# Kernel optimization log

Measured on AMD Instinct MI355X. Metric: run time of the kernel, lower is better.

## Reference

```python
import jax, jax.numpy as jnp
import numpy as np

NUM_HEADS = 32
HEAD_DIM = 128
HIDDEN = 4096
SEQ = 2048
BATCH = 1


def rotate_half(x):
    x1, x2 = jnp.split(x, 2, axis=-1)
    return jnp.concatenate((-x2, x1), axis=-1)


def rope_cos_sin(seq_len, dim, dtype=jnp.float32):
    inv_freq = 1.0 / (10000.0 ** (jnp.arange(0, dim, 2, dtype=jnp.float32) / dim))
    t = jnp.arange(seq_len, dtype=jnp.float32)
    freqs = jnp.einsum('i,j->ij', t, inv_freq)          # [S, dim/2]
    emb = jnp.concatenate((freqs, freqs), axis=-1)       # [S, dim]
    return jnp.cos(emb).astype(dtype), jnp.sin(emb).astype(dtype)


def setup_inputs() -> dict:
    key = jax.random.key(0)
    ks = jax.random.split(key, 6)
    s = 1.0 / np.sqrt(HIDDEN)
    return {
        'hidden_states': jax.random.normal(ks[0], (BATCH, SEQ, HIDDEN), jnp.float32),
        'attention_mask': jnp.ones((BATCH, SEQ), jnp.int32),
        'Wq': jax.random.normal(ks[1], (HIDDEN, HIDDEN), jnp.float32) * s,
        'Wk': jax.random.normal(ks[2], (HIDDEN, HIDDEN), jnp.float32) * s,
        'Wv': jax.random.normal(ks[3], (HIDDEN, HIDDEN), jnp.float32) * s,
        'Wo': jax.random.normal(ks[4], (HIDDEN, HIDDEN), jnp.float32) * s,
        'latent_queries': jax.random.normal(ks[5], (1, SEQ, HIDDEN), jnp.float32) * s,
    }


def reference(hidden_states, attention_mask, Wq, Wk, Wv, Wo, latent_queries):
    B, S, H = hidden_states.shape
    hd = HEAD_DIM
    scaling = hd ** -0.5

    def split_heads(x):  # [B,S,H] -> [B,nh,S,hd]
        return x.reshape(B, S, NUM_HEADS, hd).transpose(0, 2, 1, 3)

    k = split_heads(hidden_states @ Wk.T)
    v = split_heads(hidden_states @ Wv.T)

    cos, sin = rope_cos_sin(S, hd, hidden_states.dtype)  # [S,hd]
    cos = cos[None, None]
    sin = sin[None, None]
    k = k * cos + rotate_half(k) * sin  # rotated q is dead code in the original

    latents = jnp.broadcast_to(latent_queries[:, :S, :], (B, S, H))
    latent_q = split_heads(latents @ Wq.T)

    scores = jnp.einsum('bhqd,bhkd->bhqk', latent_q, k) * scaling
    mask = attention_mask[:, None, None, :] == 0
    scores = jnp.where(mask, -jnp.inf, scores)
    attn = jax.nn.softmax(scores.astype(jnp.float32), axis=-1).astype(hidden_states.dtype)
    # dropout is identity in eval mode
    out = jnp.einsum('bhqk,bhkd->bhqd', attn, v)
    out = out.transpose(0, 2, 1, 3).reshape(B, S, H)
    return out @ Wo.T
```

## Files before the change

kernel.cpp:

```cpp
#include <hip/hip_runtime.h>
#include <cstdint>
#include <type_traits>

typedef short bf16x8 __attribute__((ext_vector_type(8)));
typedef float f32x4 __attribute__((ext_vector_type(4)));

__device__ __forceinline__ ushort f2bf(float f) {
  union { float f; uint32_t u; } v; v.f = f;
  return (ushort)((v.u + 0x7fffu + ((v.u >> 16) & 1u)) >> 16);
}
__device__ __forceinline__ float bf2f(ushort u) {
  union { uint32_t u; float f; } v; v.u = ((uint32_t)u) << 16;
  return v.f;
}
__device__ __forceinline__ uint32_t pkbf(float x, float y) {
  uint32_t ux = (__float_as_uint(x) + 0x8000u) >> 16;
  uint32_t uy = (__float_as_uint(y) + 0x8000u) & 0xffff0000u;
  return ux | uy;
}

__device__ __forceinline__ void gld16(const void* g, void* l) {
  __builtin_amdgcn_global_load_lds(
      (__attribute__((address_space(1))) void*)(g),
      (__attribute__((address_space(3))) void*)(l), 16, 0, 0);
}

__device__ __forceinline__ uint4 ld8(const ushort* p) { return *(const uint4*)p; }
__device__ __forceinline__ uint4 ld8(const float* p) {
  float4 a = *(const float4*)p;
  float4 b = *(const float4*)(p + 4);
  uint4 r;
  r.x = pkbf(a.x, a.y); r.y = pkbf(a.z, a.w);
  r.z = pkbf(b.x, b.y); r.w = pkbf(b.z, b.w);
  return r;
}

__global__ __launch_bounds__(256) void cvt_bf16(
    const float* __restrict__ src, ushort* __restrict__ dst, int n8)
{
  int i = blockIdx.x * 256 + threadIdx.x;
  if (i >= n8) return;
  const float4* s = (const float4*)src;
  float4 a = s[2 * i], b = s[2 * i + 1];
  uint4 r;
  r.x = pkbf(a.x, a.y); r.y = pkbf(a.z, a.w);
  r.z = pkbf(b.x, b.y); r.w = pkbf(b.z, b.w);
  ((uint4*)dst)[i] = r;
}


#define BARw() __builtin_amdgcn_s_barrier()
#define LGKMW() do { asm volatile("s_waitcnt lgkmcnt(0)" ::: "memory"); \
                     __builtin_amdgcn_sched_barrier(0); } while (0)
#define VM6() asm volatile("s_waitcnt vmcnt(6)" ::: "memory")
#define VM0() asm volatile("s_waitcnt vmcnt(0)" ::: "memory")

__device__ __forceinline__ void stage_half8(
    const ushort* __restrict__ G, int row0, int col0,
    ushort* lds, int wave, int r4, int c8)
{
#pragma unroll
  for (int q = 0; q < 2; ++q) {
    const int si = q * 8 + wave;
    const ushort* g = G + (size_t)(row0 + (si >> 1) * 16 + r4) * 4096
                        + (col0 + (si & 1) * 32 + c8);
    gld16(g, lds + si * 512);
  }
}

__device__ __forceinline__ void read_a8(const ushort* base, int wm, int l16,
                                        int quad, bf16x8 (&a)[4][2])
{
#pragma unroll
  for (int f = 0; f < 4; ++f)
#pragma unroll
    for (int ks = 0; ks < 2; ++ks)
      a[f][ks] = *(const bf16x8*)(base + ((wm * 4 + f) * 2 + ks) * 512
                                       + l16 * 32 + quad * 8);
}

__device__ __forceinline__ void read_b8(const ushort* base, int wn, int l16,
                                        int quad, bf16x8 (&b)[2][2])
{
#pragma unroll
  for (int f = 0; f < 2; ++f)
#pragma unroll
    for (int ks = 0; ks < 2; ++ks)
      b[f][ks] = *(const bf16x8*)(base + ((wn * 2 + f) * 2 + ks) * 512
                                       + l16 * 32 + quad * 8);
}

template <int MH, int NH>
__device__ __forceinline__ void mfma_quad(const bf16x8 (&a)[4][2],
                                          const bf16x8 (&b)[2][2],
                                          f32x4 (&acc)[8][4])
{
  __builtin_amdgcn_s_setprio(1);
#pragma unroll
  for (int ks = 0; ks < 2; ++ks)
#pragma unroll
    for (int f = 0; f < 4; ++f)
#pragma unroll
      for (int g = 0; g < 2; ++g)
        acc[MH * 4 + f][NH * 2 + g] = __builtin_amdgcn_mfma_f32_16x16x32_bf16(
            a[f][ks], b[g][ks], acc[MH * 4 + f][NH * 2 + g], 0, 0, 0);
  __builtin_amdgcn_s_setprio(0);
}

__global__ __launch_bounds__(512, 2) void gemm_qkv8(
    const ushort* __restrict__ hb, const ushort* __restrict__ lb,
    const ushort* __restrict__ wkv, const ushort* __restrict__ wq,
    ushort* __restrict__ Kbf, ushort* __restrict__ Vtb, ushort* __restrict__ Qb)
{
  __shared__ __align__(16) ushort smem[65536];
#define LDSA(P, H) (smem + (P) * 32768 + (H) * 8192)
#define LDSB(P, H) (smem + (P) * 32768 + 16384 + (H) * 8192)

  const int tid  = threadIdx.x;
  const int wave = tid >> 6;
  const int lane = tid & 63;
  const int quad = lane >> 4;
  const int l16  = lane & 15;
  const int wm   = wave >> 2;
  const int wn   = wave & 3;
  const int r4   = lane >> 2;
  const int c8   = (lane & 3) * 8;

  const int bid = blockIdx.x;
  const int swz = (bid & 7) * 48 + (bid >> 3);
  const int xt  = swz % 48;
  const int m0  = (swz / 48) * 256;

  const ushort* Ag; const ushort* Bg; int n0;
  if (xt < 32) { Ag = hb; Bg = wkv; n0 = xt * 256; }
  else         { Ag = lb; Bg = wq;  n0 = (xt - 32) * 256; }

  f32x4 acc[8][4];
#pragma unroll
  for (int i = 0; i < 8; ++i)
#pragma unroll
    for (int j = 0; j < 4; ++j) acc[i][j] = {0.f, 0.f, 0.f, 0.f};

  bf16x8 a[4][2], b0[2][2], b1[2][2];

  stage_half8(Ag, m0,       0,  LDSA(0, 0), wave, r4, c8);
  stage_half8(Bg, n0,       0,  LDSB(0, 0), wave, r4, c8);
  stage_half8(Bg, n0 + 128, 0,  LDSB(0, 1), wave, r4, c8);
  stage_half8(Ag, m0 + 128, 0,  LDSA(0, 1), wave, r4, c8);
  stage_half8(Ag, m0,       64, LDSA(1, 0), wave, r4, c8);
  stage_half8(Bg, n0,       64, LDSB(1, 0), wave, r4, c8);
  stage_half8(Bg, n0 + 128, 64, LDSB(1, 1), wave, r4, c8);
  VM6();
  BARw();

#pragma unroll 1
  for (int t = 0; t < 64; t += 2) {
    read_a8(LDSA(0, 0), wm, l16, quad, a);
    read_b8(LDSB(0, 0), wn, l16, quad, b0);
    stage_half8(Ag, m0 + 128, (t + 1) * 64, LDSA(1, 1), wave, r4, c8);
    BARw(); LGKMW();
    mfma_quad<0, 0>(a, b0, acc);
    BARw();
    read_b8(LDSB(0, 1), wn, l16, quad, b1);
    if (t < 62) stage_half8(Ag, m0, (t + 2) * 64, LDSA(0, 0), wave, r4, c8);
    BARw(); LGKMW();
    mfma_quad<0, 1>(a, b1, acc);
    BARw();
    read_a8(LDSA(0, 1), wm, l16, quad, a);
    if (t < 62) stage_half8(Bg, n0, (t + 2) * 64, LDSB(0, 0), wave, r4, c8);
    BARw(); LGKMW();
    mfma_quad<1, 0>(a, b0, acc);
    BARw();
    if (t < 62) stage_half8(Bg, n0 + 128, (t + 2) * 64, LDSB(0, 1), wave, r4, c8);
    BARw(); LGKMW();
    mfma_quad<1, 1>(a, b1, acc);
    if (t < 62) VM6(); else VM0();
    BARw();

    read_a8(LDSA(1, 0), wm, l16, quad, a);
    read_b8(LDSB(1, 0), wn, l16, quad, b0);
    if (t < 62) stage_half8(Ag, m0 + 128, (t + 2) * 64, LDSA(0, 1), wave, r4, c8);
    BARw(); LGKMW();
    mfma_quad<0, 0>(a, b0, acc);
    BARw();
    read_b8(LDSB(1, 1), wn, l16, quad, b1);
    if (t < 61) stage_half8(Ag, m0, (t + 3) * 64, LDSA(1, 0), wave, r4, c8);
    BARw(); LGKMW();
    mfma_quad<0, 1>(a, b1, acc);
    BARw();
    read_a8(LDSA(1, 1), wm, l16, quad, a);
    if (t < 61) stage_half8(Bg, n0, (t + 3) * 64, LDSB(1, 0), wave, r4, c8);
    BARw(); LGKMW();
    mfma_quad<1, 0>(a, b0, acc);
    BARw();
    if (t < 61) stage_half8(Bg, n0 + 128, (t + 3) * 64, LDSB(1, 1), wave, r4, c8);
    BARw(); LGKMW();
    mfma_quad<1, 1>(a, b1, acc);
    if (t < 60) { VM6(); } else if (t < 62) { VM0(); }
    BARw();
  }

  const int route = (xt >= 32) ? 2 : (n0 >= 4096 ? 1 : 0);
#pragma unroll
  for (int fm = 0; fm < 8; ++fm) {
    const int rowb = m0 + (fm >> 2) * 128 + wm * 64 + (fm & 3) * 16 + quad * 4;
#pragma unroll
    for (int fn = 0; fn < 4; ++fn) {
      const int col = n0 + (fn >> 1) * 128 + wn * 32 + (fn & 1) * 16 + l16;
#pragma unroll
      for (int r = 0; r < 4; ++r) {
        const ushort val = f2bf(acc[fm][fn][r]);
        const int row = rowb + r;
        if (route == 0)      Kbf[(size_t)row * 4096 + col] = val;
        else if (route == 1) Vtb[(size_t)(col - 4096) * 2048 + row] = val;
        else                 Qb[(size_t)row * 4096 + col] = val;
      }
    }
  }
#undef LDSA
#undef LDSB
}

__global__ __launch_bounds__(256) void gemm_splitk(
    const ushort* __restrict__ A, const ushort* __restrict__ B,
    float* __restrict__ P)
{
  __shared__ __align__(16) ushort As[128 * 32];
  __shared__ __align__(16) ushort Bs[128 * 32];

  const int tid  = threadIdx.x;
  const int wave = tid >> 6;
  const int lane = tid & 63;
  const int quad = lane >> 4;
  const int l16  = lane & 15;
  const int m0 = blockIdx.y * 128;
  const int n0 = blockIdx.x * 128;
  const int K  = 4096;
  const int kb = blockIdx.z * 2048;

  const int wm = (wave & 1) * 64;
  const int wn = (wave >> 1) * 64;
  const int srow = lane >> 2;
  const int scol = (lane & 3) * 8;
  const ushort* ga0 = A + (size_t)(m0 + 32 * wave + srow) * K + scol + kb;
  const ushort* ga1 = ga0 + (size_t)16 * K;
  const ushort* gb0 = B + (size_t)(n0 + 32 * wave + srow) * K + scol + kb;
  const ushort* gb1 = gb0 + (size_t)16 * K;
  ushort* la0 = As + (2 * wave) * 512;
  ushort* la1 = As + (2 * wave + 1) * 512;
  ushort* lb0 = Bs + (2 * wave) * 512;
  ushort* lb1 = Bs + (2 * wave + 1) * 512;

  f32x4 acc[4][4];
#pragma unroll
  for (int i = 0; i < 4; i++)
#pragma unroll
    for (int j = 0; j < 4; j++) acc[i][j] = {0.f, 0.f, 0.f, 0.f};

  for (int k0 = 0; k0 < 2048; k0 += 32) {
    __syncthreads();
    gld16(ga0 + k0, la0);
    gld16(ga1 + k0, la1);
    gld16(gb0 + k0, lb0);
    gld16(gb1 + k0, lb1);
    __syncthreads();

    bf16x8 af[4], bfr[4];
#pragma unroll
    for (int i = 0; i < 4; i++) {
      af[i]  = *(const bf16x8*)(As + (wm + i * 16 + l16) * 32 + quad * 8);
      bfr[i] = *(const bf16x8*)(Bs + (wn + i * 16 + l16) * 32 + quad * 8);
    }
#pragma unroll
    for (int im = 0; im < 4; im++)
#pragma unroll
      for (int in = 0; in < 4; in++)
        acc[im][in] = __builtin_amdgcn_mfma_f32_16x16x32_bf16(
            af[im], bfr[in], acc[im][in], 0, 0, 0);
  }

  float* myP = P + (size_t)blockIdx.z * 2048 * 4096;
#pragma unroll
  for (int im = 0; im < 4; im++)
#pragma unroll
    for (int in = 0; in < 4; in++)
#pragma unroll
      for (int r = 0; r < 4; r++) {
        int row = m0 + wm + im * 16 + quad * 4 + r;
        int col = n0 + wn + in * 16 + l16;
        myP[(size_t)row * 4096 + col] = acc[im][in][r];
      }
}

__global__ __launch_bounds__(256) void reduce2(
    const float* __restrict__ P, float* __restrict__ out, int n4)
{
  int i = blockIdx.x * 256 + threadIdx.x;
  if (i >= n4) return;
  const float4* p0 = (const float4*)P;
  const float4* p1 = (const float4*)(P + (size_t)2048 * 4096);
  float4 a = p0[i], b = p1[i];
  float4 r; r.x = a.x + b.x; r.y = a.y + b.y; r.z = a.z + b.z; r.w = a.w + b.w;
  ((float4*)out)[i] = r;
}

template <bool TRANSC, typename TA, typename TB, typename TC>
__global__ __launch_bounds__(256) void gemm_bt(
    const TA* __restrict__ A, const TB* __restrict__ B,
    TC* __restrict__ C, int M, int N, int K, int ldc)
{
  __shared__ __align__(16) ushort As[128 * 32];
  __shared__ __align__(16) ushort Bs[128 * 32];

  const int tid  = threadIdx.x;
  const int wave = tid >> 6;
  const int lane = tid & 63;
  const int quad = lane >> 4;
  const int l16  = lane & 15;
  const int m0 = blockIdx.y * 128;
  const int n0 = blockIdx.x * 128;
  const int wm = (wave & 1) * 64;
  const int wn = (wave >> 1) * 64;
  const int r0 = tid >> 2;
  const int c0 = (tid & 3) * 8;

  f32x4 acc[4][4];
#pragma unroll
  for (int i = 0; i < 4; i++)
#pragma unroll
    for (int j = 0; j < 4; j++) acc[i][j] = {0.f, 0.f, 0.f, 0.f};

  const TA* aptr = A + (size_t)(m0 + r0) * K + c0;
  const TB* bptr = B + (size_t)(n0 + r0) * K + c0;

  for (int k0 = 0; k0 < K; k0 += 32) {
    uint4 av0 = ld8(aptr + k0);
    uint4 av1 = ld8(aptr + (size_t)64 * K + k0);
    uint4 bv0 = ld8(bptr + k0);
    uint4 bv1 = ld8(bptr + (size_t)64 * K + k0);
    __syncthreads();
    *(uint4*)(As + r0 * 32 + c0)        = av0;
    *(uint4*)(As + (r0 + 64) * 32 + c0) = av1;
    *(uint4*)(Bs + r0 * 32 + c0)        = bv0;
    *(uint4*)(Bs + (r0 + 64) * 32 + c0) = bv1;
    __syncthreads();

    bf16x8 af[4], bfr[4];
#pragma unroll
    for (int i = 0; i < 4; i++) {
      af[i]  = *(const bf16x8*)(As + (wm + i * 16 + l16) * 32 + quad * 8);
      bfr[i] = *(const bf16x8*)(Bs + (wn + i * 16 + l16) * 32 + quad * 8);
    }
#pragma unroll
    for (int im = 0; im < 4; im++)
#pragma unroll
      for (int in = 0; in < 4; in++)
        acc[im][in] = __builtin_amdgcn_mfma_f32_16x16x32_bf16(
            af[im], bfr[in], acc[im][in], 0, 0, 0);
  }

#pragma unroll
  for (int im = 0; im < 4; im++)
#pragma unroll
    for (int in = 0; in < 4; in++)
#pragma unroll
      for (int r = 0; r < 4; r++) {
        int row = m0 + wm + im * 16 + quad * 4 + r;
        int col = n0 + wn + in * 16 + l16;
        float fv = acc[im][in][r];
        TC val;
        if constexpr (std::is_same<TC, ushort>::value) val = f2bf(fv);
        else                                           val = fv;
        if (TRANSC) C[(size_t)col * ldc + row] = val;
        else        C[(size_t)row * ldc + col] = val;
      }
}

__global__ __launch_bounds__(256) void rope_kernel(ushort* __restrict__ Kb)
{
  int idx = blockIdx.x * 256 + threadIdx.x;
  int j  = idx & 63;
  int hs = idx >> 6;
  int s  = hs >> 5;
  float freq = expf(-0.14391156f * (float)j);
  float ang  = (float)s * freq;
  float sn, c;
  sincosf(ang, &sn, &c);
  size_t base = (size_t)hs * 128 + j;
  float k1 = bf2f(Kb[base]);
  float k2 = bf2f(Kb[base + 64]);
  Kb[base]      = f2bf(k1 * c - k2 * sn);
  Kb[base + 64] = f2bf(k2 * c + k1 * sn);
}

__global__ __launch_bounds__(256) void flash_attn(
    const ushort* __restrict__ Q, const ushort* __restrict__ Kb,
    const ushort* __restrict__ Vt, ushort* __restrict__ AO)
{
  __shared__ __align__(16) ushort Kt[128 * 128];
  __shared__ __align__(16) ushort Vs[128 * 128];
  __shared__ __align__(16) ushort Ps[4][16 * 128];

  const int tid  = threadIdx.x;
  const int wave = tid >> 6;
  const int lane = tid & 63;
  const int quad = lane >> 4;
  const int l16  = lane & 15;
  const int h  = blockIdx.y;
  const int q0 = blockIdx.x * 64 + wave * 16;
  const float scale = 0.08838834764831845f;

  bf16x8 aq[4];
#pragma unroll
  for (int kt = 0; kt < 4; kt++)
    aq[kt] = *(const bf16x8*)(Q + (size_t)(q0 + l16) * 4096 + h * 128 + kt * 32 + quad * 8);

  f32x4 Oacc[8];
#pragma unroll
  for (int dt = 0; dt < 8; dt++) Oacc[dt] = {0.f, 0.f, 0.f, 0.f};
  float m_i[4], l_i[4];
#pragma unroll
  for (int r = 0; r < 4; r++) { m_i[r] = -1e30f; l_i[r] = 0.f; }

  ushort* myP = &Ps[wave][0];

  for (int kv = 0; kv < 2048; kv += 128) {
    __syncthreads();
#pragma unroll
    for (int it = 0; it < 8; it++) {
      int i   = tid + it * 256;
      int row = i >> 4;
      int g   = i & 15;
      int sw  = (g ^ (row & 15)) * 8;
      *(uint4*)(Kt + row * 128 + sw) =
          *(const uint4*)(Kb + (size_t)(kv + row) * 4096 + h * 128 + g * 8);
      *(uint4*)(Vs + row * 128 + sw) =
          *(const uint4*)(Vt + (size_t)(h * 128 + row) * 2048 + kv + g * 8);
    }
    __syncthreads();

    f32x4 sA[8];
#pragma unroll
    for (int nt = 0; nt < 8; nt++) sA[nt] = {0.f, 0.f, 0.f, 0.f};
#pragma unroll
    for (int nt = 0; nt < 8; nt++) {
      int row = nt * 16 + l16;
#pragma unroll
      for (int kt = 0; kt < 4; kt++) {
        int g = kt * 4 + quad;
        bf16x8 bk = *(const bf16x8*)(Kt + row * 128 + ((g ^ (row & 15)) * 8));
        sA[nt] = __builtin_amdgcn_mfma_f32_16x16x32_bf16(aq[kt], bk, sA[nt], 0, 0, 0);
      }
    }

    float tmax[4];
#pragma unroll
    for (int r = 0; r < 4; r++) {
      float m = sA[0][r];
#pragma unroll
      for (int nt = 1; nt < 8; nt++) m = fmaxf(m, sA[nt][r]);
      tmax[r] = m;
    }
#pragma unroll
    for (int msk = 1; msk < 16; msk <<= 1)
#pragma unroll
      for (int r = 0; r < 4; r++)
        tmax[r] = fmaxf(tmax[r], __shfl_xor(tmax[r], msk));

    float alpha[4];
#pragma unroll
    for (int r = 0; r < 4; r++) {
      float mn = fmaxf(m_i[r], tmax[r] * scale);
      alpha[r] = __expf(m_i[r] - mn);
      m_i[r] = mn;
    }
    float rsum[4] = {0.f, 0.f, 0.f, 0.f};
#pragma unroll
    for (int nt = 0; nt < 8; nt++)
#pragma unroll
      for (int r = 0; r < 4; r++) {
        float p = __expf(sA[nt][r] * scale - m_i[r]);
        sA[nt][r] = p;
        rsum[r] += p;
      }
#pragma unroll
    for (int msk = 1; msk < 16; msk <<= 1)
#pragma unroll
      for (int r = 0; r < 4; r++) rsum[r] += __shfl_xor(rsum[r], msk);
#pragma unroll
    for (int r = 0; r < 4; r++) l_i[r] = l_i[r] * alpha[r] + rsum[r];

#pragma unroll
    for (int nt = 0; nt < 8; nt++)
#pragma unroll
      for (int r = 0; r < 4; r++) {
        int row = quad * 4 + r;
        int col = nt * 16 + l16;
        myP[row * 128 + (((col >> 3) ^ row) * 8) + (col & 7)] = f2bf(sA[nt][r]);
      }

#pragma unroll
    for (int dt = 0; dt < 8; dt++)
#pragma unroll
      for (int r = 0; r < 4; r++) Oacc[dt][r] *= alpha[r];

#pragma unroll
    for (int kt = 0; kt < 4; kt++) {
      int g = kt * 4 + quad;
      bf16x8 ap = *(const bf16x8*)(myP + l16 * 128 + ((g ^ l16) * 8));
#pragma unroll
      for (int dt = 0; dt < 8; dt++) {
        int vrow = dt * 16 + l16;
        bf16x8 bv = *(const bf16x8*)(Vs + vrow * 128 + ((g ^ (vrow & 15)) * 8));
        Oacc[dt] = __builtin_amdgcn_mfma_f32_16x16x32_bf16(ap, bv, Oacc[dt], 0, 0, 0);
      }
    }
  }

#pragma unroll
  for (int dt = 0; dt < 8; dt++)
#pragma unroll
    for (int r = 0; r < 4; r++) {
      int row = q0 + quad * 4 + r;
      int col = h * 128 + dt * 16 + l16;
      AO[(size_t)row * 4096 + col] = f2bf(Oacc[dt][r] / l_i[r]);
    }
}

extern "C" void kernel_launch(void* const* d_in, const int* in_sizes, int n_in,
                              void* d_out, int out_size, void* d_ws, size_t ws_size,
                              hipStream_t stream)
{
  const float* hidden  = (const float*)d_in[0];
  const float* Wq      = (const float*)d_in[2];
  const float* Wk      = (const float*)d_in[3];
  const float* Wv      = (const float*)d_in[4];
  const float* Wo      = (const float*)d_in[5];
  const float* latents = (const float*)d_in[6];
  float* out = (float*)d_out;

  const size_t SB = (size_t)2048 * 4096 * 2;
  char* w = (char*)d_ws;
  const int n8_act = 2048 * 4096 / 8;
  const int n8_wt  = 4096 * 4096 / 8;

  if (ws_size >= 13 * SB) {
    ushort* hb  = (ushort*)(w);
    ushort* lb  = (ushort*)(w + 1 * SB);
    ushort* wqb = (ushort*)(w + 2 * SB);
    ushort* wkv = (ushort*)(w + 4 * SB);
    ushort* wob = (ushort*)(w + 8 * SB);
    ushort* Qb  = (ushort*)(w + 10 * SB);
    ushort* Kbf = (ushort*)(w + 11 * SB);
    ushort* Vtb = (ushort*)(w + 12 * SB);
    ushort* AOb = wqb;
    float*  Pp  = (float*)(w + 4 * SB);

    cvt_bf16<<<n8_act / 256, 256, 0, stream>>>(hidden,  hb,  n8_act);
    cvt_bf16<<<n8_act / 256, 256, 0, stream>>>(latents, lb,  n8_act);
    cvt_bf16<<<n8_wt / 256, 256, 0, stream>>>(Wq, wqb, n8_wt);
    cvt_bf16<<<n8_wt / 256, 256, 0, stream>>>(Wk, wkv, n8_wt);
    cvt_bf16<<<n8_wt / 256, 256, 0, stream>>>(Wv, wkv + (size_t)4096 * 4096, n8_wt);
    cvt_bf16<<<n8_wt / 256, 256, 0, stream>>>(Wo, wob, n8_wt);

    gemm_qkv8<<<dim3(384), 512, 0, stream>>>(hb, lb, wkv, wqb, Kbf, Vtb, Qb);
    rope_kernel<<<(2048 * 32 * 64) / 256, 256, 0, stream>>>(Kbf);
    flash_attn<<<dim3(32, 32), 256, 0, stream>>>(Qb, Kbf, Vtb, AOb);
    gemm_splitk<<<dim3(32, 16, 2), 256, 0, stream>>>(AOb, wob, Pp);
    reduce2<<<(2048 * 4096 / 4 + 255) / 256, 256, 0, stream>>>(Pp, out, 2048 * 4096 / 4);
  } else {
    ushort* Qb  = (ushort*)(w);
    ushort* Kbf = (ushort*)(w + 1 * SB);
    ushort* Vtb = (ushort*)(w + 2 * SB);
    ushort* AOb = (ushort*)(w + 3 * SB);

    gemm_bt<false><<<dim3(32, 16), 256, 0, stream>>>(latents, Wq, Qb, 2048, 4096, 4096, 4096);
    gemm_bt<false><<<dim3(32, 16), 256, 0, stream>>>(hidden, Wk, Kbf, 2048, 4096, 4096, 4096);
    gemm_bt<true><<<dim3(32, 16), 256, 0, stream>>>(hidden, Wv, Vtb, 2048, 4096, 4096, 2048);
    rope_kernel<<<(2048 * 32 * 64) / 256, 256, 0, stream>>>(Kbf);
    flash_attn<<<dim3(32, 32), 256, 0, stream>>>(Qb, Kbf, Vtb, AOb);
    gemm_bt<false><<<dim3(32, 16), 256, 0, stream>>>(AOb, Wo, out, 2048, 4096, 4096, 4096);
  }
}
```

Baseline: 949.9 us.

## Reuse pipelined 256x256 GEMM for output projection and restructure flash attention

The fused QKV GEMM kernel is templated on K-iterations and mode so the output projection's split-K GEMM uses the same deep-pipelined 256x256 tile kernel instead of the simple 128x128 one. Flash attention moves to 512-thread blocks covering 128 queries and prefetches the next K/V tile into registers while computing the current one. It also raises MFMA priority and applies the lazy rescale trick, rescaling the running max and accumulators only when the max grows by more than a threshold. These changes target low MFMA utilisation and exposed global-load latency, at the cost of higher register pressure and fewer blocks for the output GEMM.

```diff
diff --git a/kernel.cpp b/kernel.cpp
--- a/kernel.cpp
+++ b/kernel.cpp
@@ -107,10 +107,12 @@
   __builtin_amdgcn_s_setprio(0);
 }
 
-__global__ __launch_bounds__(512, 2) void gemm_qkv8(
-    const ushort* __restrict__ hb, const ushort* __restrict__ lb,
-    const ushort* __restrict__ wkv, const ushort* __restrict__ wq,
-    ushort* __restrict__ Kbf, ushort* __restrict__ Vtb, ushort* __restrict__ Qb)
+template <int NT, int MODE>
+__global__ __launch_bounds__(512, 2) void gemm8(
+    const ushort* __restrict__ A0, const ushort* __restrict__ A1,
+    const ushort* __restrict__ B0, const ushort* __restrict__ B1,
+    ushort* __restrict__ O0, ushort* __restrict__ O1, ushort* __restrict__ O2,
+    float* __restrict__ PF)
 {
   __shared__ __align__(16) ushort smem[65536];
 #define LDSA(P, H) (smem + (P) * 32768 + (H) * 8192)
@@ -127,13 +129,24 @@
   const int c8   = (lane & 3) * 8;
 
   const int bid = blockIdx.x;
-  const int swz = (bid & 7) * 48 + (bid >> 3);
-  const int xt  = swz % 48;
-  const int m0  = (swz / 48) * 256;
-
-  const ushort* Ag; const ushort* Bg; int n0;
-  if (xt < 32) { Ag = hb; Bg = wkv; n0 = xt * 256; }
-  else         { Ag = lb; Bg = wq;  n0 = (xt - 32) * 256; }
+  const ushort* Ag; const ushort* Bg;
+  int m0, n0, kbase = 0, route = 0, kz = 0;
+  if constexpr (MODE == 0) {
+    const int swz = (bid & 7) * 48 + (bid >> 3);
+    const int xt  = swz % 48;
+    m0 = (swz / 48) * 256;
+    if (xt < 32) { Ag = A0; Bg = B0; n0 = xt * 256; }
+    else         { Ag = A1; Bg = B1; n0 = (xt - 32) * 256; }
+    route = (xt >= 32) ? 2 : (n0 >= 4096 ? 1 : 0);
+  } else {
+    const int swz = (bid & 7) * 32 + (bid >> 3);
+    kz = swz >> 7;
+    const int r = swz & 127;
+    m0 = (r >> 4) * 256;
+    n0 = (r & 15) * 256;
+    kbase = kz * 2048;
+    Ag = A0; Bg = B0;
+  }
 
   f32x4 acc[8][4];
 #pragma unroll
@@ -143,153 +156,102 @@
 
   bf16x8 a[4][2], b0[2][2], b1[2][2];
 
-  stage_half8(Ag, m0,       0,  LDSA(0, 0), wave, r4, c8);
-  stage_half8(Bg, n0,       0,  LDSB(0, 0), wave, r4, c8);
-  stage_half8(Bg, n0 + 128, 0,  LDSB(0, 1), wave, r4, c8);
-  stage_half8(Ag, m0 + 128, 0,  LDSA(0, 1), wave, r4, c8);
-  stage_half8(Ag, m0,       64, LDSA(1, 0), wave, r4, c8);
-  stage_half8(Bg, n0,       64, LDSB(1, 0), wave, r4, c8);
-  stage_half8(Bg, n0 + 128, 64, LDSB(1, 1), wave, r4, c8);
+  stage_half8(Ag, m0,       kbase,      LDSA(0, 0), wave, r4, c8);
+  stage_half8(Bg, n0,       kbase,      LDSB(0, 0), wave, r4, c8);
+  stage_half8(Bg, n0 + 128, kbase,      LDSB(0, 1), wave, r4, c8);
+  stage_half8(Ag, m0 + 128, kbase,      LDSA(0, 1), wave, r4, c8);
+  stage_half8(Ag, m0,       kbase + 64, LDSA(1, 0), wave, r4, c8);
+  stage_half8(Bg, n0,       kbase + 64, LDSB(1, 0), wave, r4, c8);
+  stage_half8(Bg, n0 + 128, kbase + 64, LDSB(1, 1), wave, r4, c8);
   VM6();
   BARw();
 
 #pragma unroll 1
-  for (int t = 0; t < 64; t += 2) {
+  for (int t = 0; t < NT; t += 2) {
     read_a8(LDSA(0, 0), wm, l16, quad, a);
     read_b8(LDSB(0, 0), wn, l16, quad, b0);
-    stage_half8(Ag, m0 + 128, (t + 1) * 64, LDSA(1, 1), wave, r4, c8);
+    stage_half8(Ag, m0 + 128, kbase + (t + 1) * 64, LDSA(1, 1), wave, r4, c8);
     BARw(); LGKMW();
     mfma_quad<0, 0>(a, b0, acc);
     BARw();
+
     read_b8(LDSB(0, 1), wn, l16, quad, b1);
-    if (t < 62) stage_half8(Ag, m0, (t + 2) * 64, LDSA(0, 0), wave, r4, c8);
+    if (t < NT - 2) stage_half8(Ag, m0, kbase + (t + 2) * 64, LDSA(0, 0), wave, r4, c8);
     BARw(); LGKMW();
     mfma_quad<0, 1>(a, b1, acc);
     BARw();
+
     read_a8(LDSA(0, 1), wm, l16, quad, a);
-    if (t < 62) stage_half8(Bg, n0, (t + 2) * 64, LDSB(0, 0), wave, r4, c8);
+    if (t < NT - 2) stage_half8(Bg, n0, kbase + (t + 2) * 64, LDSB(0, 0), wave, r4, c8);
     BARw(); LGKMW();
     mfma_quad<1, 0>(a, b0, acc);
     BARw();
-    if (t < 62) stage_half8(Bg, n0 + 128, (t + 2) * 64, LDSB(0, 1), wave, r4, c8);
+
+    if (t < NT - 2) stage_half8(Bg, n0 + 128, kbase + (t + 2) * 64, LDSB(0, 1), wave, r4, c8);
     BARw(); LGKMW();
     mfma_quad<1, 1>(a, b1, acc);
-    if (t < 62) VM6(); else VM0();
+    if (t < NT - 2) VM6(); else VM0();
     BARw();
 
     read_a8(LDSA(1, 0), wm, l16, quad, a);
     read_b8(LDSB(1, 0), wn, l16, quad, b0);
-    if (t < 62) stage_half8(Ag, m0 + 128, (t + 2) * 64, LDSA(0, 1), wave, r4, c8);
+    if (t < NT - 2) stage_half8(Ag, m0 + 128, kbase + (t + 2) * 64, LDSA(0, 1), wave, r4, c8);
     BARw(); LGKMW();
     mfma_quad<0, 0>(a, b0, acc);
     BARw();
+
     read_b8(LDSB(1, 1), wn, l16, quad, b1);
-    if (t < 61) stage_half8(Ag, m0, (t + 3) * 64, LDSA(1, 0), wave, r4, c8);
+    if (t < NT - 3) stage_half8(Ag, m0, kbase + (t + 3) * 64, LDSA(1, 0), wave, r4, c8);
     BARw(); LGKMW();
     mfma_quad<0, 1>(a, b1, acc);
     BARw();
+
     read_a8(LDSA(1, 1), wm, l16, quad, a);
-    if (t < 61) stage_half8(Bg, n0, (t + 3) * 64, LDSB(1, 0), wave, r4, c8);
+    if (t < NT - 3) stage_half8(Bg, n0, kbase + (t + 3) * 64, LDSB(1, 0), wave, r4, c8);
     BARw(); LGKMW();
     mfma_quad<1, 0>(a, b0, acc);
     BARw();
-    if (t < 61) stage_half8(Bg, n0 + 128, (t + 3) * 64, LDSB(1, 1), wave, r4, c8);
+
+    if (t < NT - 3) stage_half8(Bg, n0 + 128, kbase + (t + 3) * 64, LDSB(1, 1), wave, r4, c8);
     BARw(); LGKMW();
     mfma_quad<1, 1>(a, b1, acc);
-    if (t < 60) { VM6(); } else if (t < 62) { VM0(); }
-    BARw();
-  }
-
-  const int route = (xt >= 32) ? 2 : (n0 >= 4096 ? 1 : 0);
-#pragma unroll
-  for (int fm = 0; fm < 8; ++fm) {
-    const int rowb = m0 + (fm >> 2) * 128 + wm * 64 + (fm & 3) * 16 + quad * 4;
-#pragma unroll
-    for (int fn = 0; fn < 4; ++fn) {
-      const int col = n0 + (fn >> 1) * 128 + wn * 32 + (fn & 1) * 16 + l16;
-#pragma unroll
-      for (int r = 0; r < 4; ++r) {
-        const ushort val = f2bf(acc[fm][fn][r]);
-        const int row = rowb + r;
-        if (route == 0)      Kbf[(size_t)row * 4096 + col] = val;
-        else if (route == 1) Vtb[(size_t)(col - 4096) * 2048 + row] = val;
-        else                 Qb[(size_t)row * 4096 + col] = val;
+    if (t < NT - 4) { VM6(); } else if (t < NT - 2) { VM0(); }
+    BARw();
+  }
+
+  if constexpr (MODE == 0) {
+#pragma unroll
+    for (int fm = 0; fm < 8; ++fm) {
+      const int rowb = m0 + (fm >> 2) * 128 + wm * 64 + (fm & 3) * 16 + quad * 4;
+#pragma unroll
+      for (int fn = 0; fn < 4; ++fn) {
+        const int col = n0 + (fn >> 1) * 128 + wn * 32 + (fn & 1) * 16 + l16;
+#pragma unroll
+        for (int r = 0; r < 4; ++r) {
+          const ushort val = f2bf(acc[fm][fn][r]);
+          const int row = rowb + r;
+          if (route == 0)      O0[(size_t)row * 4096 + col] = val;
+          else if (route == 1) O1[(size_t)(col - 4096) * 2048 + row] = val;
+          else                 O2[(size_t)row * 4096 + col] = val;
+        }
+      }
+    }
+  } else {
+    float* myP = PF + (size_t)kz * 2048 * 4096;
+#pragma unroll
+    for (int fm = 0; fm < 8; ++fm) {
+      const int rowb = m0 + (fm >> 2) * 128 + wm * 64 + (fm & 3) * 16 + quad * 4;
+#pragma unroll
+      for (int fn = 0; fn < 4; ++fn) {
+        const int col = n0 + (fn >> 1) * 128 + wn * 32 + (fn & 1) * 16 + l16;
+#pragma unroll
+        for (int r = 0; r < 4; ++r)
+          myP[(size_t)(rowb + r) * 4096 + col] = acc[fm][fn][r];
       }
     }
   }
 #undef LDSA
 #undef LDSB
-}
-
-__global__ __launch_bounds__(256) void gemm_splitk(
-    const ushort* __restrict__ A, const ushort* __restrict__ B,
-    float* __restrict__ P)
-{
-  __shared__ __align__(16) ushort As[128 * 32];
-  __shared__ __align__(16) ushort Bs[128 * 32];
-
-  const int tid  = threadIdx.x;
-  const int wave = tid >> 6;
-  const int lane = tid & 63;
-  const int quad = lane >> 4;
-  const int l16  = lane & 15;
-  const int m0 = blockIdx.y * 128;
-  const int n0 = blockIdx.x * 128;
-  const int K  = 4096;
-  const int kb = blockIdx.z * 2048;
-
-  const int wm = (wave & 1) * 64;
-  const int wn = (wave >> 1) * 64;
-  const int srow = lane >> 2;
-  const int scol = (lane & 3) * 8;
-  const ushort* ga0 = A + (size_t)(m0 + 32 * wave + srow) * K + scol + kb;
-  const ushort* ga1 = ga0 + (size_t)16 * K;
-  const ushort* gb0 = B + (size_t)(n0 + 32 * wave + srow) * K + scol + kb;
-  const ushort* gb1 = gb0 + (size_t)16 * K;
-  ushort* la0 = As + (2 * wave) * 512;
-  ushort* la1 = As + (2 * wave + 1) * 512;
-  ushort* lb0 = Bs + (2 * wave) * 512;
-  ushort* lb1 = Bs + (2 * wave + 1) * 512;
-
-  f32x4 acc[4][4];
-#pragma unroll
-  for (int i = 0; i < 4; i++)
-#pragma unroll
-    for (int j = 0; j < 4; j++) acc[i][j] = {0.f, 0.f, 0.f, 0.f};
-
-  for (int k0 = 0; k0 < 2048; k0 += 32) {
-    __syncthreads();
-    gld16(ga0 + k0, la0);
-    gld16(ga1 + k0, la1);
-    gld16(gb0 + k0, lb0);
-    gld16(gb1 + k0, lb1);
-    __syncthreads();
-
-    bf16x8 af[4], bfr[4];
-#pragma unroll
-    for (int i = 0; i < 4; i++) {
-      af[i]  = *(const bf16x8*)(As + (wm + i * 16 + l16) * 32 + quad * 8);
-      bfr[i] = *(const bf16x8*)(Bs + (wn + i * 16 + l16) * 32 + quad * 8);
-    }
-#pragma unroll
-    for (int im = 0; im < 4; im++)
-#pragma unroll
-      for (int in = 0; in < 4; in++)
-        acc[im][in] = __builtin_amdgcn_mfma_f32_16x16x32_bf16(
-            af[im], bfr[in], acc[im][in], 0, 0, 0);
-  }
-
-  float* myP = P + (size_t)blockIdx.z * 2048 * 4096;
-#pragma unroll
-  for (int im = 0; im < 4; im++)
-#pragma unroll
-    for (int in = 0; in < 4; in++)
-#pragma unroll
-      for (int r = 0; r < 4; r++) {
-        int row = m0 + wm + im * 16 + quad * 4 + r;
-        int col = n0 + wn + in * 16 + l16;
-        myP[(size_t)row * 4096 + col] = acc[im][in][r];
-      }
 }
 
 __global__ __launch_bounds__(256) void reduce2(
@@ -393,13 +355,13 @@
   Kb[base + 64] = f2bf(k2 * c + k1 * sn);
 }
 
-__global__ __launch_bounds__(256) void flash_attn(
+__global__ __launch_bounds__(512, 2) void flash_attn(
     const ushort* __restrict__ Q, const ushort* __restrict__ Kb,
     const ushort* __restrict__ Vt, ushort* __restrict__ AO)
 {
   __shared__ __align__(16) ushort Kt[128 * 128];
   __shared__ __align__(16) ushort Vs[128 * 128];
-  __shared__ __align__(16) ushort Ps[4][16 * 128];
+  __shared__ __align__(16) ushort Ps[8][16 * 128];
 
   const int tid  = threadIdx.x;
   const int wave = tid >> 6;
@@ -407,7 +369,7 @@
   const int quad = lane >> 4;
   const int l16  = lane & 15;
   const int h  = blockIdx.y;
-  const int q0 = blockIdx.x * 64 + wave * 16;
+  const int q0 = blockIdx.x * 128 + wave * 16;
   const float scale = 0.08838834764831845f;
 
   bf16x8 aq[4];
@@ -424,24 +386,41 @@
 
   ushort* myP = &Ps[wave][0];
 
+  uint4 kr[4], vr[4];
+#pragma unroll
+  for (int it = 0; it < 4; ++it) {
+    int i = tid + it * 512;
+    int row = i >> 4, g = i & 15;
+    kr[it] = *(const uint4*)(Kb + (size_t)row * 4096 + h * 128 + g * 8);
+    vr[it] = *(const uint4*)(Vt + (size_t)(h * 128 + row) * 2048 + g * 8);
+  }
+
   for (int kv = 0; kv < 2048; kv += 128) {
     __syncthreads();
 #pragma unroll
-    for (int it = 0; it < 8; it++) {
-      int i   = tid + it * 256;
-      int row = i >> 4;
-      int g   = i & 15;
-      int sw  = (g ^ (row & 15)) * 8;
-      *(uint4*)(Kt + row * 128 + sw) =
-          *(const uint4*)(Kb + (size_t)(kv + row) * 4096 + h * 128 + g * 8);
-      *(uint4*)(Vs + row * 128 + sw) =
-          *(const uint4*)(Vt + (size_t)(h * 128 + row) * 2048 + kv + g * 8);
+    for (int it = 0; it < 4; ++it) {
+      int i = tid + it * 512;
+      int row = i >> 4, g = i & 15;
+      int sw = (g ^ (row & 15)) * 8;
+      *(uint4*)(Kt + row * 128 + sw) = kr[it];
+      *(uint4*)(Vs + row * 128 + sw) = vr[it];
     }
     __syncthreads();
 
+    if (kv + 128 < 2048) {
+#pragma unroll
+      for (int it = 0; it < 4; ++it) {
+        int i = tid + it * 512;
+        int row = i >> 4, g = i & 15;
+        kr[it] = *(const uint4*)(Kb + (size_t)(kv + 128 + row) * 4096 + h * 128 + g * 8);
+        vr[it] = *(const uint4*)(Vt + (size_t)(h * 128 + row) * 2048 + kv + 128 + g * 8);
+      }
+    }
+
     f32x4 sA[8];
 #pragma unroll
     for (int nt = 0; nt < 8; nt++) sA[nt] = {0.f, 0.f, 0.f, 0.f};
+    __builtin_amdgcn_s_setprio(1);
 #pragma unroll
     for (int nt = 0; nt < 8; nt++) {
       int row = nt * 16 + l16;
@@ -452,6 +431,7 @@
         sA[nt] = __builtin_amdgcn_mfma_f32_16x16x32_bf16(aq[kt], bk, sA[nt], 0, 0, 0);
       }
     }
+    __builtin_amdgcn_s_setprio(0);
 
     float tmax[4];
 #pragma unroll
@@ -467,13 +447,25 @@
       for (int r = 0; r < 4; r++)
         tmax[r] = fmaxf(tmax[r], __shfl_xor(tmax[r], msk));
 
-    float alpha[4];
+    float nm[4];
+    float growth = -1e30f;
 #pragma unroll
     for (int r = 0; r < 4; r++) {
-      float mn = fmaxf(m_i[r], tmax[r] * scale);
-      alpha[r] = __expf(m_i[r] - mn);
-      m_i[r] = mn;
-    }
+      nm[r] = tmax[r] * scale;
+      growth = fmaxf(growth, nm[r] - m_i[r]);
+    }
+    if (__any(growth > 8.0f)) {
+#pragma unroll
+      for (int r = 0; r < 4; r++) {
+        float mn = fmaxf(m_i[r], nm[r]);
+        float al = __expf(m_i[r] - mn);
+        m_i[r] = mn;
+        l_i[r] *= al;
+#pragma unroll
+        for (int dt = 0; dt < 8; dt++) Oacc[dt][r] *= al;
+      }
+    }
+
     float rsum[4] = {0.f, 0.f, 0.f, 0.f};
 #pragma unroll
     for (int nt = 0; nt < 8; nt++)
@@ -488,7 +480,7 @@
 #pragma unroll
       for (int r = 0; r < 4; r++) rsum[r] += __shfl_xor(rsum[r], msk);
 #pragma unroll
-    for (int r = 0; r < 4; r++) l_i[r] = l_i[r] * alpha[r] + rsum[r];
+    for (int r = 0; r < 4; r++) l_i[r] += rsum[r];
 
 #pragma unroll
     for (int nt = 0; nt < 8; nt++)
@@ -499,11 +491,7 @@
         myP[row * 128 + (((col >> 3) ^ row) * 8) + (col & 7)] = f2bf(sA[nt][r]);
       }
 
-#pragma unroll
-    for (int dt = 0; dt < 8; dt++)
-#pragma unroll
-      for (int r = 0; r < 4; r++) Oacc[dt][r] *= alpha[r];
-
+    __builtin_amdgcn_s_setprio(1);
 #pragma unroll
     for (int kt = 0; kt < 4; kt++) {
       int g = kt * 4 + quad;
@@ -515,6 +503,7 @@
         Oacc[dt] = __builtin_amdgcn_mfma_f32_16x16x32_bf16(ap, bv, Oacc[dt], 0, 0, 0);
       }
     }
+    __builtin_amdgcn_s_setprio(0);
   }
 
 #pragma unroll
@@ -563,10 +552,11 @@
     cvt_bf16<<<n8_wt / 256, 256, 0, stream>>>(Wv, wkv + (size_t)4096 * 4096, n8_wt);
     cvt_bf16<<<n8_wt / 256, 256, 0, stream>>>(Wo, wob, n8_wt);
 
-    gemm_qkv8<<<dim3(384), 512, 0, stream>>>(hb, lb, wkv, wqb, Kbf, Vtb, Qb);
+    gemm8<64, 0><<<dim3(384), 512, 0, stream>>>(hb, lb, wkv, wqb, Kbf, Vtb, Qb, nullptr);
     rope_kernel<<<(2048 * 32 * 64) / 256, 256, 0, stream>>>(Kbf);
-    flash_attn<<<dim3(32, 32), 256, 0, stream>>>(Qb, Kbf, Vtb, AOb);
-    gemm_splitk<<<dim3(32, 16, 2), 256, 0, stream>>>(AOb, wob, Pp);
+    flash_attn<<<dim3(16, 32), 512, 0, stream>>>(Qb, Kbf, Vtb, AOb);
+    gemm8<32, 1><<<dim3(256), 512, 0, stream>>>(AOb, AOb, wob, wob,
+                                                nullptr, nullptr, nullptr, Pp);
     reduce2<<<(2048 * 4096 / 4 + 255) / 256, 256, 0, stream>>>(Pp, out, 2048 * 4096 / 4);
   } else {
     ushort* Qb  = (ushort*)(w);
@@ -578,7 +568,7 @@
     gemm_bt<false><<<dim3(32, 16), 256, 0, stream>>>(hidden, Wk, Kbf, 2048, 4096, 4096, 4096);
     gemm_bt<true><<<dim3(32, 16), 256, 0, stream>>>(hidden, Wv, Vtb, 2048, 4096, 4096, 2048);
     rope_kernel<<<(2048 * 32 * 64) / 256, 256, 0, stream>>>(Kbf);
-    flash_attn<<<dim3(32, 32), 256, 0, stream>>>(Qb, Kbf, Vtb, AOb);
+    flash_attn<<<dim3(16, 32), 512, 0, stream>>>(Qb, Kbf, Vtb, AOb);
     gemm_bt<false><<<dim3(32, 16), 256, 0, stream>>>(AOb, Wo, out, 2048, 4096, 4096, 4096);
   }
 }
```

Result: faster. 841.0 us (-11.5%).
